# Performance work log

Measured on AMD Instinct MI355X. Metric: run time of the kernel, lower is better.

The kernel has to match this reference:

```python
import jax, jax.numpy as jnp
import numpy as np
import math

B, T, E, H = 8, 1024, 768, 12
D = E // H  # 64

def setup_inputs() -> dict:
    key = jax.random.key(0)
    ks = jax.random.split(key, 5)
    return {
        "x": jax.random.normal(ks[0], (B, T, E), dtype=jnp.float32),
        "w_attn": jax.random.normal(ks[1], (E, 3 * E), dtype=jnp.float32) * 0.02,
        "b_attn": jax.random.normal(ks[2], (3 * E,), dtype=jnp.float32) * 0.02,
        "w_proj": jax.random.normal(ks[3], (E, E), dtype=jnp.float32) * 0.02,
        "b_proj": jax.random.normal(ks[4], (E,), dtype=jnp.float32) * 0.02,
    }

def reference(x, w_attn, b_attn, w_proj, b_proj):
    b, t, e = x.shape
    h, d = H, E // H
    qkv = x @ w_attn + b_attn                      # [B,T,3E]
    q, k, v = jnp.split(qkv, 3, axis=2)
    q = q.reshape(b, t, h, d).transpose(0, 2, 1, 3)  # [B,H,T,D]
    k = k.reshape(b, t, h, d).transpose(0, 2, 1, 3)
    v = v.reshape(b, t, h, d).transpose(0, 2, 1, 3)
    scores = jnp.einsum('bhqd,bhkd->bhqk', q, k)     # [B,H,T,T]
    causal = jnp.tril(jnp.ones((t, t), dtype=bool))
    scores = jnp.where(causal[None, None], scores, -jnp.inf)
    attn = jax.nn.softmax(scores / jnp.float32(math.sqrt(d)), axis=-1)
    out = jnp.einsum('bhqk,bhkd->bhqd', attn, v)     # [B,H,T,D]
    out = out.transpose(0, 2, 1, 3).reshape(b, t, h * d)
    return out @ w_proj + b_proj
```

## Files before the change

### kernel.cpp

```cpp
#include <hip/hip_runtime.h>
#include <math.h>


#define B_ 8
#define T_ 1024
#define E_ 768
#define H_ 12
#define D_ 64
#define E3 (3 * E_)

typedef __attribute__((ext_vector_type(8))) short bf16x8;
typedef __attribute__((ext_vector_type(4))) float f32x4;

#define SCALE 0.18033688f

__device__ __forceinline__ unsigned short f2bf(float f) {
    unsigned int u = __builtin_bit_cast(unsigned int, f);
    u += 0x7fffu + ((u >> 16) & 1u);
    return (unsigned short)(u >> 16);
}

__device__ __forceinline__ void async_copy16(void* lds, const void* g) {
    __builtin_amdgcn_global_load_lds(
        (const __attribute__((address_space(1))) void*)g,
        (__attribute__((address_space(3))) void*)lds, 16, 0, 0);
}

#define NCVT 6144
#define NTA  (72 * 24)
#define NTP  (24 * 24)

__device__ __forceinline__ void transpose_tile(
    const float* __restrict__ W, unsigned short* __restrict__ Wt,
    int K, int N, int gx, int gy, unsigned short (*tile)[33])
{
    const int n0 = gx * 32, k0 = gy * 32;
    const int tx = threadIdx.x & 31, ty = threadIdx.x >> 5;
    #pragma unroll
    for (int i = 0; i < 4; ++i)
        tile[ty + i * 8][tx] = f2bf(W[(size_t)(k0 + ty + i * 8) * N + n0 + tx]);
    __syncthreads();
    #pragma unroll
    for (int i = 0; i < 4; ++i)
        Wt[(size_t)(n0 + ty + i * 8) * K + k0 + tx] = tile[tx][ty + i * 8];
}

__global__ __launch_bounds__(256) void prep_kernel(
    const float* __restrict__ x, unsigned short* __restrict__ x_bf,
    const float* __restrict__ w_attn, unsigned short* __restrict__ wat,
    const float* __restrict__ w_proj, unsigned short* __restrict__ wpt)
{
    __shared__ unsigned short tile[32][33];
    const int bid = blockIdx.x;
    if (bid < NCVT) {
        const int i = bid * 256 + threadIdx.x;
        float4 f = ((const float4*)x)[i];
        ushort4 o;
        o.x = f2bf(f.x); o.y = f2bf(f.y); o.z = f2bf(f.z); o.w = f2bf(f.w);
        ((ushort4*)x_bf)[i] = o;
    } else if (bid < NCVT + NTA) {
        const int t = bid - NCVT;
        transpose_tile(w_attn, wat, E_, E3, t % 72, t / 72, tile);
    } else {
        const int t = bid - NCVT - NTA;
        transpose_tile(w_proj, wpt, E_, E_, t % 24, t / 24, tile);
    }
}


__global__ __launch_bounds__(512, 2) void gemm_qkv_256(
    const unsigned short* __restrict__ A,
    const unsigned short* __restrict__ Wt,
    const float* __restrict__ bias,
    unsigned short* __restrict__ C,
    unsigned short* __restrict__ vt)
{
    constexpr int K = 768;
    constexpr int N = E3;
    constexpr int NI = 6;

    extern __shared__ unsigned short lds[];
    unsigned short* const Ab0 = lds;
    unsigned short* const Ab1 = lds + 16384;
    unsigned short* const Bb0 = lds + 32768;
    unsigned short* const Bb1 = lds + 49152;

    const int tid  = threadIdx.x;
    const int lane = tid & 63;
    const int w    = tid >> 6;
    const int wm   = w >> 2;
    const int wn   = w & 3;
    const int n16  = lane & 15;
    const int quad = lane >> 4;
    const int l7   = lane & 7;
    const int lrow = lane >> 3;
    const int lcol = (l7 ^ lrow) * 8;

    const int lin  = blockIdx.x;
    const int work = (lin & 7) * 36 + (lin >> 3);
    const int by = work / 9, bx = work % 9;
    const int bm = by * 256, bn = bx * 256;

    const unsigned short* Asrc = A  + (size_t)(bm + w * 16 + lrow) * K + lcol;
    const unsigned short* Bsrc = Wt + (size_t)(bn + w * 16 + lrow) * K + lcol;

    auto stgA = [&](unsigned short* buf, int kt, int h) {
        #pragma unroll
        for (int i = 0; i < 2; ++i)
            async_copy16(&buf[h * 8192 + (w * 2 + i) * 512],
                         Asrc + (size_t)(h * 128 + i * 8) * K + kt * 64);
    };
    auto stgB = [&](unsigned short* buf, int kt, int h) {
        #pragma unroll
        for (int i = 0; i < 2; ++i)
            async_copy16(&buf[h * 8192 + (w * 2 + i) * 512],
                         Bsrc + (size_t)(h * 128 + i * 8) * K + kt * 64);
    };

    bf16x8 afr[8], b0f[4], b1f[4];
    f32x4 acc[8][4] = {};

#define LDA(buf, qm) { \
    _Pragma("unroll") \
    for (int ml = 0; ml < 4; ++ml) { \
        const int r = wm * 16 + ((qm) * 4 + ml) * 32 + n16; \
        const unsigned short* rp = (buf) + r * 64; \
        afr[ml * 2 + 0] = *(const bf16x8*)&rp[((0 + quad) ^ l7) * 8]; \
        afr[ml * 2 + 1] = *(const bf16x8*)&rp[((4 + quad) ^ l7) * 8]; \
    } }
#define LDB(bfr, buf, qn) { \
    _Pragma("unroll") \
    for (int nl = 0; nl < 2; ++nl) { \
        const int r = wn * 16 + ((qn) * 2 + nl) * 64 + n16; \
        const unsigned short* rp = (buf) + r * 64; \
        bfr[nl * 2 + 0] = *(const bf16x8*)&rp[((0 + quad) ^ l7) * 8]; \
        bfr[nl * 2 + 1] = *(const bf16x8*)&rp[((4 + quad) ^ l7) * 8]; \
    } }
#define MM(qm, qn, bfr) { \
    _Pragma("unroll") \
    for (int ml = 0; ml < 4; ++ml) \
    _Pragma("unroll") \
    for (int nl = 0; nl < 2; ++nl) \
    _Pragma("unroll") \
    for (int kk = 0; kk < 2; ++kk) \
        acc[(qm) * 4 + ml][(qn) * 2 + nl] = __builtin_amdgcn_mfma_f32_16x16x32_bf16( \
            afr[ml * 2 + kk], bfr[nl * 2 + kk], acc[(qm) * 4 + ml][(qn) * 2 + nl], 0, 0, 0); }

#define BARR  __builtin_amdgcn_s_barrier()
#define LGKM0 asm volatile("s_waitcnt lgkmcnt(0)" ::: "memory")
#define VM6   asm volatile("s_waitcnt vmcnt(6)" ::: "memory")
#define VM0   asm volatile("s_waitcnt vmcnt(0)" ::: "memory")
#define PRI1  __builtin_amdgcn_s_setprio(1)
#define PRI0  __builtin_amdgcn_s_setprio(0)

    stgA(Ab0, 0, 0); stgB(Bb0, 0, 0); stgB(Bb0, 0, 1); stgA(Ab0, 0, 1);
    stgA(Ab1, 1, 0); stgB(Bb1, 1, 0); stgB(Bb1, 1, 1);
    VM6; BARR;

    #pragma unroll 1
    for (int I = 0; I < NI - 1; ++I) {
        const int u = 2 * I;
        LDA(Ab0, 0); LDB(b0f, Bb0, 0);
        stgA(Ab1, u + 1, 1);
        BARR; LGKM0; PRI1; MM(0, 0, b0f); PRI0; BARR;
        LDB(b1f, Bb0, 1);
        stgA(Ab0, u + 2, 0);
        BARR; LGKM0; PRI1; MM(0, 1, b1f); PRI0; BARR;
        LDA(Ab0, 1);
        stgB(Bb0, u + 2, 0);
        BARR; LGKM0; PRI1; MM(1, 1, b1f); PRI0; BARR;
        stgB(Bb0, u + 2, 1);
        BARR; LGKM0; PRI1; MM(1, 0, b0f); PRI0; VM6; BARR;
        LDA(Ab1, 0); LDB(b0f, Bb1, 0);
        stgA(Ab0, u + 2, 1);
        BARR; LGKM0; PRI1; MM(0, 0, b0f); PRI0; BARR;
        LDB(b1f, Bb1, 1);
        stgA(Ab1, u + 3, 0);
        BARR; LGKM0; PRI1; MM(0, 1, b1f); PRI0; BARR;
        LDA(Ab1, 1);
        stgB(Bb1, u + 3, 0);
        BARR; LGKM0; PRI1; MM(1, 1, b1f); PRI0; BARR;
        stgB(Bb1, u + 3, 1);
        BARR; LGKM0; PRI1; MM(1, 0, b0f); PRI0; VM6; BARR;
    }

    LDA(Ab0, 0); LDB(b0f, Bb0, 0);
    stgA(Ab1, 11, 1);
    BARR; LGKM0; PRI1; MM(0, 0, b0f); PRI0; BARR;
    LDB(b1f, Bb0, 1);
    BARR; LGKM0; PRI1; MM(0, 1, b1f); PRI0; BARR;
    LDA(Ab0, 1);
    BARR; LGKM0; PRI1; MM(1, 1, b1f); PRI0; BARR;
    BARR; PRI1; MM(1, 0, b0f); PRI0; VM0; BARR;
    LDA(Ab1, 0); LDB(b0f, Bb1, 0);
    BARR; LGKM0; PRI1; MM(0, 0, b0f); PRI0; BARR;
    LDB(b1f, Bb1, 1);
    BARR; LGKM0; PRI1; MM(0, 1, b1f); PRI0; BARR;
    LDA(Ab1, 1);
    BARR; LGKM0; PRI1; MM(1, 1, b1f); PRI0; BARR;
    PRI1; MM(1, 0, b0f); PRI0;

#undef LDA
#undef LDB
#undef MM

    if (bx >= 6) {
        #pragma unroll
        for (int m = 0; m < 8; ++m) {
            const int tt = bm + wm * 16 + m * 32 + quad * 4;
            const size_t bb = (size_t)(tt >> 10) * 768;
            const int tin = tt & 1023;
            #pragma unroll
            for (int n = 0; n < 4; ++n) {
                const int col = bn + wn * 16 + n * 64 + n16;
                const int ch = col - 1536;
                const float bv = bias[col];
                ushort4 o4;
                o4.x = f2bf(acc[m][n][0] + bv);
                o4.y = f2bf(acc[m][n][1] + bv);
                o4.z = f2bf(acc[m][n][2] + bv);
                o4.w = f2bf(acc[m][n][3] + bv);
                *(ushort4*)&vt[(bb + ch) * 1024 + tin] = o4;
            }
        }
    } else {
        const bool scale_q = bx < 3;
        #pragma unroll
        for (int m = 0; m < 8; ++m) {
            #pragma unroll
            for (int r = 0; r < 4; ++r) {
                const size_t rowoff = (size_t)(bm + wm * 16 + m * 32 + quad * 4 + r) * N;
                #pragma unroll
                for (int n = 0; n < 4; ++n) {
                    const int col = bn + wn * 16 + n * 64 + n16;
                    float v = acc[m][n][r] + bias[col];
                    if (scale_q) v *= SCALE;
                    C[rowoff + col] = f2bf(v);
                }
            }
        }
    }
}

template <typename OutT, int MODE, int BM, int BN, int WR, int WC>
__global__ __launch_bounds__(256) void gemm_mfma_kernel(
    const unsigned short* __restrict__ A,
    const unsigned short* __restrict__ Wt,
    const float* __restrict__ bias,
    OutT* __restrict__ C,
    unsigned short* __restrict__ vt,
    int M, int N, int K)
{
    constexpr int MT = BM / WR / 16;
    constexpr int NT = BN / WC / 16;
    constexpr int CA = BM / 32;
    constexpr int CB = BN / 32;
    constexpr int QBX = 768 / BN;
    constexpr int VBX = 1536 / BN;

    __shared__ unsigned short Abuf[BM * 64];
    __shared__ unsigned short Bbuf[BN * 64];

    const int tid = threadIdx.x;
    const int lane = tid & 63;
    const int w = tid >> 6;
    const int n16 = lane & 15;
    const int quad = lane >> 4;

    const int nbx = gridDim.x;
    const int lin = blockIdx.y * nbx + blockIdx.x;
    const int band_sz = 8 * nbx;
    const int band = lin / band_sz;
    const int rr = lin % band_sz;
    const int bm = (band * 8 + (rr & 7)) * BM;
    const int bx = rr >> 3;
    const int bn = bx * BN;

    const int wmbase = (w / WC) * (BM / WR);
    const int wnbase = (w % WC) * (BN / WC);

    const int lrow = lane >> 3;
    const int lcol = ((lane & 7) ^ lrow) * 8;

    f32x4 acc[MT][NT] = {};

    for (int k0 = 0; k0 < K; k0 += 64) {
        __syncthreads();
        #pragma unroll
        for (int i = 0; i < CA; ++i) {
            const int c = w * CA + i;
            const int row = c * 8 + lrow;
            async_copy16(&Abuf[c * 512], A + (size_t)(bm + row) * K + k0 + lcol);
        }
        #pragma unroll
        for (int i = 0; i < CB; ++i) {
            const int c = w * CB + i;
            const int row = c * 8 + lrow;
            async_copy16(&Bbuf[c * 512], Wt + (size_t)(bn + row) * K + k0 + lcol);
        }
        __syncthreads();

        #pragma unroll
        for (int kc = 0; kc < 2; ++kc) {
            bf16x8 af[MT], bf[NT];
            #pragma unroll
            for (int mt = 0; mt < MT; ++mt) {
                const int r = wmbase + mt * 16 + n16;
                af[mt] = *(const bf16x8*)&Abuf[r * 64 + ((kc * 4 + quad) ^ (r & 7)) * 8];
            }
            #pragma unroll
            for (int nt = 0; nt < NT; ++nt) {
                const int r = wnbase + nt * 16 + n16;
                bf[nt] = *(const bf16x8*)&Bbuf[r * 64 + ((kc * 4 + quad) ^ (r & 7)) * 8];
            }
            #pragma unroll
            for (int mt = 0; mt < MT; ++mt)
                #pragma unroll
                for (int nt = 0; nt < NT; ++nt)
                    acc[mt][nt] = __builtin_amdgcn_mfma_f32_16x16x32_bf16(
                        af[mt], bf[nt], acc[mt][nt], 0, 0, 0);
        }
    }

    if (MODE == 1 && bx >= VBX) {
        #pragma unroll
        for (int mt = 0; mt < MT; ++mt) {
            const int tt = bm + wmbase + mt * 16 + quad * 4;
            const size_t bb = (size_t)(tt >> 10) * 768;
            const int tin = tt & 1023;
            #pragma unroll
            for (int nt = 0; nt < NT; ++nt) {
                const int col = bn + wnbase + nt * 16 + n16;
                const int ch = col - 1536;
                const float bv = bias[col];
                ushort4 o4;
                o4.x = f2bf(acc[mt][nt][0] + bv);
                o4.y = f2bf(acc[mt][nt][1] + bv);
                o4.z = f2bf(acc[mt][nt][2] + bv);
                o4.w = f2bf(acc[mt][nt][3] + bv);
                *(ushort4*)&vt[(bb + ch) * 1024 + tin] = o4;
            }
        }
        return;
    }

    const bool scale_q = (MODE == 1) && (bx < QBX);
    #pragma unroll
    for (int mt = 0; mt < MT; ++mt) {
        #pragma unroll
        for (int r = 0; r < 4; ++r) {
            const size_t rowoff = (size_t)(bm + wmbase + mt * 16 + quad * 4 + r) * N;
            #pragma unroll
            for (int nt = 0; nt < NT; ++nt) {
                const int col = bn + wnbase + nt * 16 + n16;
                float v = acc[mt][nt][r] + bias[col];
                if (scale_q) v *= SCALE;
                if constexpr (sizeof(OutT) == 2) C[rowoff + col] = (OutT)f2bf(v);
                else                             C[rowoff + col] = (OutT)v;
            }
        }
    }
}

#define BKEY 128
#define VSTR 136

__global__ __launch_bounds__(256) void flash_attn_kernel(
    const unsigned short* __restrict__ qkv,
    const unsigned short* __restrict__ vt,
    unsigned short* __restrict__ out)
{
    __shared__ unsigned short Ks[BKEY * 64];
    __shared__ unsigned short Vts[64 * BKEY];
    __shared__ unsigned short Ps[4 * 16 * VSTR];

    const int tid = threadIdx.x;
    const int idx = blockIdx.x;
    const int head = idx % 96;
    const int p    = idx / 96;
    const int h = head % H_;
    const int b = head / H_;

    const int lane = tid & 63;
    const int w    = tid >> 6;
    const int n16  = lane & 15;
    const int quad = lane >> 4;

    const size_t base = (size_t)b * T_ * E3;
    const unsigned short* qbase = qkv + base + h * D_;
    const unsigned short* kbase = qkv + base + E_ + h * D_;
    const unsigned short* vtb   = vt + (size_t)(b * H_ + h) * 64 * 1024;

    const int lrow = lane >> 3;
    const int lcol = ((lane & 7) ^ lrow) * 8;
    const int vr4 = lane >> 4;
    const int vc  = lane & 15;

    unsigned short* pw = &Ps[w * 16 * VSTR];

    const int qtA = p, qtB = 15 - p;
    const int nIterA = (qtA + 2) >> 1;
    const int nIterB = (qtB + 2) >> 1;
    const int wqA = qtA * 64 + w * 16;
    const int wqB = qtB * 64 + w * 16;

    const unsigned short* qrpA = qbase + (size_t)(wqA + n16) * E3 + quad * 8;
    bf16x8 qfA0 = *(const bf16x8*)qrpA;
    bf16x8 qfA1 = *(const bf16x8*)(qrpA + 32);
    const unsigned short* qrpB = qbase + (size_t)(wqB + n16) * E3 + quad * 8;
    bf16x8 qfB0 = *(const bf16x8*)qrpB;
    bf16x8 qfB1 = *(const bf16x8*)(qrpB + 32);

    f32x4 oA[4] = {}, oB[4] = {};
    float lsA = 0.f, lsB = 0.f;

    for (int it = 0; it < nIterB; ++it) {
        const int k0 = it * BKEY;
        __syncthreads();

        #pragma unroll
        for (int i = 0; i < 4; ++i) {
            const int c = w * 4 + i;
            const int row = c * 8 + lrow;
            async_copy16(&Ks[c * 512], kbase + (size_t)(k0 + row) * E3 + lcol);
        }
        #pragma unroll
        for (int i = 0; i < 4; ++i) {
            const int j = w * 4 + i;
            const int row = 4 * j + vr4;
            async_copy16(&Vts[4 * j * BKEY],
                         vtb + (size_t)row * 1024 + k0 + ((vc ^ (row & 15)) * 8));
        }
        __syncthreads();

        auto phase = [&](bf16x8 qf0, bf16x8 qf1, f32x4* o, float& lsum,
                         int wave_q_min) {
            int knt_lim = ((wave_q_min + 15 - k0) >> 4) + 1;
            if (knt_lim > 8) knt_lim = 8;
            const int ks_lim = (knt_lim + 1) >> 1;
            int Ab2 = wave_q_min - k0 - 15;
            int kfull = Ab2 < 0 ? 0 : (Ab2 >> 4) + 1;
            if (kfull > 8) kfull = 8;

            const int qcol = wave_q_min + n16;

            f32x4 s[8];
            #pragma unroll
            for (int knt = 0; knt < 8; ++knt) {
                if (knt < knt_lim) {
                    const int r = knt * 16 + n16;
                    bf16x8 kf0 = *(const bf16x8*)&Ks[r * 64 + ((0 + quad) ^ (r & 7)) * 8];
                    bf16x8 kf1 = *(const bf16x8*)&Ks[r * 64 + ((4 + quad) ^ (r & 7)) * 8];
                    f32x4 acc = {0.f, 0.f, 0.f, 0.f};
                    acc = __builtin_amdgcn_mfma_f32_16x16x32_bf16(kf0, qf0, acc, 0, 0, 0);
                    acc = __builtin_amdgcn_mfma_f32_16x16x32_bf16(kf1, qf1, acc, 0, 0, 0);
                    s[knt] = acc;
                }
            }
            #pragma unroll
            for (int knt = 0; knt < 8; ++knt) {
                if (knt >= kfull) {
                    const int krow = k0 + knt * 16 + quad * 4;
                    #pragma unroll
                    for (int r = 0; r < 4; ++r) {
                        float v = (knt < knt_lim) ? s[knt][r] : -1e30f;
                        if (krow + r > qcol) v = -1e30f;
                        s[knt][r] = v;
                    }
                }
            }

            #pragma unroll
            for (int knt = 0; knt < 8; ++knt) {
                float pv0 = __builtin_amdgcn_exp2f(s[knt][0]);
                float pv1 = __builtin_amdgcn_exp2f(s[knt][1]);
                float pv2 = __builtin_amdgcn_exp2f(s[knt][2]);
                float pv3 = __builtin_amdgcn_exp2f(s[knt][3]);
                lsum += (pv0 + pv1) + (pv2 + pv3);
                unsigned int u0 = __builtin_bit_cast(unsigned int, pv0);
                unsigned int u1 = __builtin_bit_cast(unsigned int, pv1);
                unsigned int u2 = __builtin_bit_cast(unsigned int, pv2);
                unsigned int u3 = __builtin_bit_cast(unsigned int, pv3);
                uint2 pk;
                pk.x = ((u0 + 0x8000u) >> 16) | ((u1 + 0x8000u) & 0xffff0000u);
                pk.y = ((u2 + 0x8000u) >> 16) | ((u3 + 0x8000u) & 0xffff0000u);
                *(uint2*)&pw[n16 * VSTR + knt * 16 + quad * 4] = pk;
            }

            #pragma unroll
            for (int ks = 0; ks < 4; ++ks) {
                if (ks < ks_lim) {
                    bf16x8 pf = *(const bf16x8*)&pw[n16 * VSTR + ks * 32 + quad * 8];
                    #pragma unroll
                    for (int dt = 0; dt < 4; ++dt) {
                        const int row = dt * 16 + n16;
                        bf16x8 vf = *(const bf16x8*)&Vts[row * BKEY +
                                        (((ks * 4 + quad) ^ n16) * 8)];
                        o[dt] = __builtin_amdgcn_mfma_f32_16x16x32_bf16(pf, vf, o[dt], 0, 0, 0);
                    }
                }
            }
        };

        phase(qfB0, qfB1, oB, lsB, wqB);
        if (it < nIterA) phase(qfA0, qfA1, oA, lsA, wqA);
    }

    lsA += __shfl_xor(lsA, 16); lsA += __shfl_xor(lsA, 32);
    lsB += __shfl_xor(lsB, 16); lsB += __shfl_xor(lsB, 32);

    #pragma unroll
    for (int r = 0; r < 4; ++r) {
        const float invA = 1.f / __shfl(lsA, quad * 4 + r);
        unsigned short* orowA = out + ((size_t)b * T_ + wqA + quad * 4 + r) * E_ + h * D_;
        #pragma unroll
        for (int dt = 0; dt < 4; ++dt)
            orowA[dt * 16 + n16] = f2bf(oA[dt][r] * invA);
        const float invB = 1.f / __shfl(lsB, quad * 4 + r);
        unsigned short* orowB = out + ((size_t)b * T_ + wqB + quad * 4 + r) * E_ + h * D_;
        #pragma unroll
        for (int dt = 0; dt < 4; ++dt)
            orowB[dt * 16 + n16] = f2bf(oB[dt][r] * invB);
    }
}

extern "C" void kernel_launch(void* const* d_in, const int* in_sizes, int n_in,
                              void* d_out, int out_size, void* d_ws, size_t ws_size,
                              hipStream_t stream)
{
    const float* x      = (const float*)d_in[0];
    const float* w_attn = (const float*)d_in[1];
    const float* b_attn = (const float*)d_in[2];
    const float* w_proj = (const float*)d_in[3];
    const float* b_proj = (const float*)d_in[4];
    float* out = (float*)d_out;

    const int M = B_ * T_;

    unsigned short* x_bf   = (unsigned short*)d_ws;
    unsigned short* wat    = x_bf + (size_t)M * E_;
    unsigned short* wpt    = wat + (size_t)E3 * E_;
    unsigned short* qkv_bf = wpt + (size_t)E_ * E_;
    unsigned short* att_bf = qkv_bf + (size_t)M * E3;
    unsigned short* vt_bf  = att_bf + (size_t)M * E_;

    static bool qkv_attr_set = false;
    if (!qkv_attr_set) {
        hipFuncSetAttribute((const void*)gemm_qkv_256,
                            hipFuncAttributeMaxDynamicSharedMemorySize, 131072);
        qkv_attr_set = true;
    }

    prep_kernel<<<NCVT + NTA + NTP, 256, 0, stream>>>(x, x_bf, w_attn, wat, w_proj, wpt);

    gemm_qkv_256<<<dim3(288), dim3(512), 131072, stream>>>(
        x_bf, wat, b_attn, qkv_bf, vt_bf);

    flash_attn_kernel<<<B_ * H_ * 8, 256, 0, stream>>>(qkv_bf, vt_bf, att_bf);

    gemm_mfma_kernel<float, 0, 64, 128, 2, 2>
        <<<dim3(E_ / 128, M / 64), 256, 0, stream>>>(
        att_bf, wpt, b_proj, out, nullptr, M, E_, E_);
}
```

Measured before the change: 200.4 us.

## Prefetch next K/V tile into registers during attention compute; remap blocks per XCD

Replaces the async global-to-LDS copies in the flash attention loop with register prefetch of the next K/V tile, issued before the current tile's compute and written to LDS after a barrier. This is meant to hide global load latency behind the MFMA work. Blocks are also remapped so each XCD processes a contiguous group of heads, which should improve L2 reuse of K/V. The launch bounds now request 3 blocks per SM, and the extra prefetch registers add register pressure.

```diff
diff --git a/kernel.cpp b/kernel.cpp
--- a/kernel.cpp
+++ b/kernel.cpp
@@ -66,7 +66,6 @@
         transpose_tile(w_proj, wpt, E_, E_, t % 24, t / 24, tile);
     }
 }
-
 
 __global__ __launch_bounds__(512, 2) void gemm_qkv_256(
     const unsigned short* __restrict__ A,
@@ -365,19 +364,21 @@
 #define BKEY 128
 #define VSTR 136
 
-__global__ __launch_bounds__(256) void flash_attn_kernel(
+__global__ __launch_bounds__(256, 3) void flash_attn_kernel(
     const unsigned short* __restrict__ qkv,
     const unsigned short* __restrict__ vt,
     unsigned short* __restrict__ out)
 {
-    __shared__ unsigned short Ks[BKEY * 64];
-    __shared__ unsigned short Vts[64 * BKEY];
-    __shared__ unsigned short Ps[4 * 16 * VSTR];
+    __shared__ __align__(16) unsigned short Ks[BKEY * 64];
+    __shared__ __align__(16) unsigned short Vts[64 * BKEY];
+    __shared__ __align__(16) unsigned short Ps[4 * 16 * VSTR];
 
     const int tid = threadIdx.x;
     const int idx = blockIdx.x;
-    const int head = idx % 96;
-    const int p    = idx / 96;
+    const int xcd = idx & 7;
+    const int j   = idx >> 3;
+    const int head = xcd * 12 + (j % 12);
+    const int p    = j / 12;
     const int h = head % H_;
     const int b = head / H_;
 
@@ -414,24 +415,39 @@
     f32x4 oA[4] = {}, oB[4] = {};
     float lsA = 0.f, lsB = 0.f;
 
-    for (int it = 0; it < nIterB; ++it) {
-        const int k0 = it * BKEY;
-        __syncthreads();
-
+    uint4 kreg[4], vreg[4];
+    auto load_tile = [&](int k0) {
         #pragma unroll
         for (int i = 0; i < 4; ++i) {
             const int c = w * 4 + i;
             const int row = c * 8 + lrow;
-            async_copy16(&Ks[c * 512], kbase + (size_t)(k0 + row) * E3 + lcol);
+            kreg[i] = *(const uint4*)(kbase + (size_t)(k0 + row) * E3 + lcol);
         }
         #pragma unroll
         for (int i = 0; i < 4; ++i) {
-            const int j = w * 4 + i;
-            const int row = 4 * j + vr4;
-            async_copy16(&Vts[4 * j * BKEY],
-                         vtb + (size_t)row * 1024 + k0 + ((vc ^ (row & 15)) * 8));
-        }
-        __syncthreads();
+            const int jj = w * 4 + i;
+            const int row = 4 * jj + vr4;
+            vreg[i] = *(const uint4*)(vtb + (size_t)row * 1024 + k0 +
+                                      ((vc ^ (row & 15)) * 8));
+        }
+    };
+    auto write_tile = [&]() {
+        #pragma unroll
+        for (int i = 0; i < 4; ++i)
+            *(uint4*)((char*)Ks + (size_t)(w * 4 + i) * 1024 + lane * 16) = kreg[i];
+        #pragma unroll
+        for (int i = 0; i < 4; ++i)
+            *(uint4*)((char*)Vts + (size_t)(w * 4 + i) * 1024 + lane * 16) = vreg[i];
+    };
+
+    load_tile(0);
+    write_tile();
+    __syncthreads();
+
+    for (int it = 0; it < nIterB; ++it) {
+        const int k0 = it * BKEY;
+        const bool pre = (it + 1 < nIterB);
+        if (pre) load_tile(k0 + BKEY);
 
         auto phase = [&](bf16x8 qf0, bf16x8 qf1, f32x4* o, float& lsum,
                          int wave_q_min) {
@@ -504,6 +520,12 @@
 
         phase(qfB0, qfB1, oB, lsB, wqB);
         if (it < nIterA) phase(qfA0, qfA1, oA, lsA, wqA);
+
+        __syncthreads();
+        if (pre) {
+            write_tile();
+        }
+        __syncthreads();
     }
 
     lsA += __shfl_xor(lsA, 16); lsA += __shfl_xor(lsA, 32);
```

Result: slower. 215.2 us (+7.4%).

## Double-buffer K tiles, pass P via shuffles, and remap blocks per XCD

Applied to the files above, without the earlier changes.

The flash-attention kernel now double-buffers K in LDS and prefetches the next K tile while the current QK^T and softmax run. The V tile load is overlapped with score computation using partial vmcnt waits and a mid-phase barrier. The P matrix is kept in registers and rearranged with cross-lane shuffles instead of a round trip through LDS, which removes the Ps buffer. Block indices are remapped so each XCD handles a contiguous set of heads for better L2 locality, and launch bounds now request 3 blocks per CU. The shuffles add ALU and permute work, and the hand-written waitcnt counts depend on the exact number of outstanding loads.

```diff
diff --git a/kernel.cpp b/kernel.cpp
--- a/kernel.cpp
+++ b/kernel.cpp
@@ -66,7 +66,6 @@
         transpose_tile(w_proj, wpt, E_, E_, t % 24, t / 24, tile);
     }
 }
-
 
 __global__ __launch_bounds__(512, 2) void gemm_qkv_256(
     const unsigned short* __restrict__ A,
@@ -363,21 +362,21 @@
 }
 
 #define BKEY 128
-#define VSTR 136
-
-__global__ __launch_bounds__(256) void flash_attn_kernel(
+
+__global__ __launch_bounds__(256, 3) void flash_attn_kernel(
     const unsigned short* __restrict__ qkv,
     const unsigned short* __restrict__ vt,
     unsigned short* __restrict__ out)
 {
-    __shared__ unsigned short Ks[BKEY * 64];
-    __shared__ unsigned short Vts[64 * BKEY];
-    __shared__ unsigned short Ps[4 * 16 * VSTR];
+    __shared__ __align__(16) unsigned short Ks[2][BKEY * 64];
+    __shared__ __align__(16) unsigned short Vts[64 * BKEY];
 
     const int tid = threadIdx.x;
     const int idx = blockIdx.x;
-    const int head = idx % 96;
-    const int p    = idx / 96;
+    const int xcd = idx & 7;
+    const int j   = idx >> 3;
+    const int head = xcd * 12 + (j % 12);
+    const int p    = j / 12;
     const int h = head % H_;
     const int b = head / H_;
 
@@ -395,8 +394,6 @@
     const int lcol = ((lane & 7) ^ lrow) * 8;
     const int vr4 = lane >> 4;
     const int vc  = lane & 15;
-
-    unsigned short* pw = &Ps[w * 16 * VSTR];
 
     const int qtA = p, qtB = 15 - p;
     const int nIterA = (qtA + 2) >> 1;
@@ -414,64 +411,74 @@
     f32x4 oA[4] = {}, oB[4] = {};
     float lsA = 0.f, lsB = 0.f;
 
-    for (int it = 0; it < nIterB; ++it) {
-        const int k0 = it * BKEY;
-        __syncthreads();
-
+    const int sLo = n16 + 32 * (quad & 1);
+    const int sHi = sLo + 16;
+    const bool hiSel = quad >= 2;
+
+    auto stageK = [&](int t) {
+        unsigned short* dst = Ks[t & 1];
+        const int k0 = t * BKEY;
         #pragma unroll
         for (int i = 0; i < 4; ++i) {
             const int c = w * 4 + i;
             const int row = c * 8 + lrow;
-            async_copy16(&Ks[c * 512], kbase + (size_t)(k0 + row) * E3 + lcol);
-        }
+            async_copy16(&dst[c * 512], kbase + (size_t)(k0 + row) * E3 + lcol);
+        }
+    };
+    auto stageV = [&](int t) {
+        const int k0 = t * BKEY;
         #pragma unroll
         for (int i = 0; i < 4; ++i) {
-            const int j = w * 4 + i;
-            const int row = 4 * j + vr4;
-            async_copy16(&Vts[4 * j * BKEY],
+            const int jj = w * 4 + i;
+            const int row = 4 * jj + vr4;
+            async_copy16(&Vts[4 * jj * BKEY],
                          vtb + (size_t)row * 1024 + k0 + ((vc ^ (row & 15)) * 8));
         }
-        __syncthreads();
-
-        auto phase = [&](bf16x8 qf0, bf16x8 qf1, f32x4* o, float& lsum,
-                         int wave_q_min) {
-            int knt_lim = ((wave_q_min + 15 - k0) >> 4) + 1;
-            if (knt_lim > 8) knt_lim = 8;
-            const int ks_lim = (knt_lim + 1) >> 1;
-            int Ab2 = wave_q_min - k0 - 15;
-            int kfull = Ab2 < 0 ? 0 : (Ab2 >> 4) + 1;
-            if (kfull > 8) kfull = 8;
-
-            const int qcol = wave_q_min + n16;
-
-            f32x4 s[8];
-            #pragma unroll
-            for (int knt = 0; knt < 8; ++knt) {
-                if (knt < knt_lim) {
-                    const int r = knt * 16 + n16;
-                    bf16x8 kf0 = *(const bf16x8*)&Ks[r * 64 + ((0 + quad) ^ (r & 7)) * 8];
-                    bf16x8 kf1 = *(const bf16x8*)&Ks[r * 64 + ((4 + quad) ^ (r & 7)) * 8];
-                    f32x4 acc = {0.f, 0.f, 0.f, 0.f};
-                    acc = __builtin_amdgcn_mfma_f32_16x16x32_bf16(kf0, qf0, acc, 0, 0, 0);
-                    acc = __builtin_amdgcn_mfma_f32_16x16x32_bf16(kf1, qf1, acc, 0, 0, 0);
-                    s[knt] = acc;
+    };
+
+    auto phase = [&](bf16x8 qf0, bf16x8 qf1, f32x4* o, float& lsum,
+                     int wave_q_min, int k0, const unsigned short* Kb,
+                     bool doMid, bool notLast) {
+        int knt_lim = ((wave_q_min + 15 - k0) >> 4) + 1;
+        if (knt_lim > 8) knt_lim = 8;
+        const int ks_lim = (knt_lim + 1) >> 1;
+        const int nkp = ks_lim * 2;
+        int Ab2 = wave_q_min - k0 - 15;
+        int kfull = Ab2 < 0 ? 0 : (Ab2 >> 4) + 1;
+        if (kfull > 8) kfull = 8;
+
+        const int qcol = wave_q_min + n16;
+
+        f32x4 s[8];
+        #pragma unroll
+        for (int knt = 0; knt < 8; ++knt) {
+            if (knt < knt_lim) {
+                const int r = knt * 16 + n16;
+                bf16x8 kf0 = *(const bf16x8*)&Kb[r * 64 + ((0 + quad) ^ (r & 7)) * 8];
+                bf16x8 kf1 = *(const bf16x8*)&Kb[r * 64 + ((4 + quad) ^ (r & 7)) * 8];
+                f32x4 acc = {0.f, 0.f, 0.f, 0.f};
+                acc = __builtin_amdgcn_mfma_f32_16x16x32_bf16(kf0, qf0, acc, 0, 0, 0);
+                acc = __builtin_amdgcn_mfma_f32_16x16x32_bf16(kf1, qf1, acc, 0, 0, 0);
+                s[knt] = acc;
+            }
+        }
+        #pragma unroll
+        for (int knt = 0; knt < 8; ++knt) {
+            if (knt >= kfull && knt < nkp) {
+                const int krow = k0 + knt * 16 + quad * 4;
+                #pragma unroll
+                for (int r = 0; r < 4; ++r) {
+                    float v = (knt < knt_lim) ? s[knt][r] : -1e30f;
+                    if (krow + r > qcol) v = -1e30f;
+                    s[knt][r] = v;
                 }
             }
-            #pragma unroll
-            for (int knt = 0; knt < 8; ++knt) {
-                if (knt >= kfull) {
-                    const int krow = k0 + knt * 16 + quad * 4;
-                    #pragma unroll
-                    for (int r = 0; r < 4; ++r) {
-                        float v = (knt < knt_lim) ? s[knt][r] : -1e30f;
-                        if (krow + r > qcol) v = -1e30f;
-                        s[knt][r] = v;
-                    }
-                }
-            }
-
-            #pragma unroll
-            for (int knt = 0; knt < 8; ++knt) {
+        }
+
+        unsigned int e0[8], e1[8];
+        #pragma unroll
+        for (int knt = 0; knt < 8; ++knt) {
+            if (knt < nkp) {
                 float pv0 = __builtin_amdgcn_exp2f(s[knt][0]);
                 float pv1 = __builtin_amdgcn_exp2f(s[knt][1]);
                 float pv2 = __builtin_amdgcn_exp2f(s[knt][2]);
@@ -481,29 +488,64 @@
                 unsigned int u1 = __builtin_bit_cast(unsigned int, pv1);
                 unsigned int u2 = __builtin_bit_cast(unsigned int, pv2);
                 unsigned int u3 = __builtin_bit_cast(unsigned int, pv3);
-                uint2 pk;
-                pk.x = ((u0 + 0x8000u) >> 16) | ((u1 + 0x8000u) & 0xffff0000u);
-                pk.y = ((u2 + 0x8000u) >> 16) | ((u3 + 0x8000u) & 0xffff0000u);
-                *(uint2*)&pw[n16 * VSTR + knt * 16 + quad * 4] = pk;
-            }
-
-            #pragma unroll
-            for (int ks = 0; ks < 4; ++ks) {
-                if (ks < ks_lim) {
-                    bf16x8 pf = *(const bf16x8*)&pw[n16 * VSTR + ks * 32 + quad * 8];
-                    #pragma unroll
-                    for (int dt = 0; dt < 4; ++dt) {
-                        const int row = dt * 16 + n16;
-                        bf16x8 vf = *(const bf16x8*)&Vts[row * BKEY +
-                                        (((ks * 4 + quad) ^ n16) * 8)];
-                        o[dt] = __builtin_amdgcn_mfma_f32_16x16x32_bf16(pf, vf, o[dt], 0, 0, 0);
-                    }
+                e0[knt] = ((u0 + 0x8000u) >> 16) | ((u1 + 0x8000u) & 0xffff0000u);
+                e1[knt] = ((u2 + 0x8000u) >> 16) | ((u3 + 0x8000u) & 0xffff0000u);
+            }
+        }
+
+        if (doMid) {
+            if (notLast) asm volatile("s_waitcnt vmcnt(4)" ::: "memory");
+            else         asm volatile("s_waitcnt vmcnt(0)" ::: "memory");
+            __builtin_amdgcn_s_barrier();
+        }
+
+        #pragma unroll
+        for (int ks = 0; ks < 4; ++ks) {
+            if (ks < ks_lim) {
+                const int kA = 2 * ks, kB = 2 * ks + 1;
+                unsigned int a0 = (unsigned)__shfl((int)e0[kA], sLo);
+                unsigned int a1 = (unsigned)__shfl((int)e1[kA], sLo);
+                unsigned int a2 = (unsigned)__shfl((int)e0[kA], sHi);
+                unsigned int a3 = (unsigned)__shfl((int)e1[kA], sHi);
+                unsigned int b0 = (unsigned)__shfl((int)e0[kB], sLo);
+                unsigned int b1 = (unsigned)__shfl((int)e1[kB], sLo);
+                unsigned int b2 = (unsigned)__shfl((int)e0[kB], sHi);
+                unsigned int b3 = (unsigned)__shfl((int)e1[kB], sHi);
+                uint4 pu;
+                pu.x = hiSel ? b0 : a0;
+                pu.y = hiSel ? b1 : a1;
+                pu.z = hiSel ? b2 : a2;
+                pu.w = hiSel ? b3 : a3;
+                bf16x8 pf = __builtin_bit_cast(bf16x8, pu);
+                #pragma unroll
+                for (int dt = 0; dt < 4; ++dt) {
+                    const int row = dt * 16 + n16;
+                    bf16x8 vf = *(const bf16x8*)&Vts[row * BKEY +
+                                    (((ks * 4 + quad) ^ n16) * 8)];
+                    o[dt] = __builtin_amdgcn_mfma_f32_16x16x32_bf16(pf, vf, o[dt], 0, 0, 0);
                 }
             }
-        };
-
-        phase(qfB0, qfB1, oB, lsB, wqB);
-        if (it < nIterA) phase(qfA0, qfA1, oA, lsA, wqA);
+        }
+    };
+
+    stageK(0);
+    asm volatile("s_waitcnt vmcnt(0)" ::: "memory");
+    __builtin_amdgcn_s_barrier();
+
+    for (int it = 0; it < nIterB; ++it) {
+        const int k0 = it * BKEY;
+        const bool notLast = (it + 1 < nIterB);
+
+        stageV(it);
+        if (notLast) stageK(it + 1);
+        const unsigned short* Kb = Ks[it & 1];
+
+        phase(qfB0, qfB1, oB, lsB, wqB, k0, Kb, true,  notLast);
+        if (it < nIterA)
+            phase(qfA0, qfA1, oA, lsA, wqA, k0, Kb, false, notLast);
+
+        asm volatile("s_waitcnt vmcnt(0)" ::: "memory");
+        __builtin_amdgcn_s_barrier();
     }
 
     lsA += __shfl_xor(lsA, 16); lsA += __shfl_xor(lsA, 32);
```

After: 186.5 us. -6.9%, faster.
